# Kernel tuning notes

Hardware: AMD Instinct MI355X
Metric: run time of the kernel (lower is better)

## Reference

```python
import jax, jax.numpy as jnp
import numpy as np

LAYERS = 3  # LightGCN propagation depth per graph


def lgconv(h, edge_index, n_nodes):
    """PyG LGConv: symmetric-normalized aggregation, no self-loops."""
    src, dst = edge_index[0], edge_index[1]
    deg = jax.ops.segment_sum(jnp.ones(dst.shape[0], h.dtype), dst, num_segments=n_nodes)
    dinv = jnp.where(deg > 0, jax.lax.rsqrt(jnp.maximum(deg, 1e-12)), 0.0).astype(h.dtype)
    norm = dinv[src] * dinv[dst]                 # [E]
    msg = h[src] * norm[:, None]                 # [E, D]
    return jax.ops.segment_sum(msg, dst, num_segments=n_nodes)


def setup_inputs() -> dict:
    key = jax.random.key(0)
    ks = jax.random.split(key, 8)
    N, D, E, B, U = 100000, 64, 1200000, 4096, 20000
    return {
        "user": jax.random.randint(ks[0], (B,), 0, U),
        "item": jax.random.randint(ks[1], (B,), 0, N),
        "x": jnp.arange(N),
        "edge_index_0": jax.random.randint(ks[2], (2, E), 0, N),
        "edge_index_1": jax.random.randint(ks[3], (2, E), 0, N),
        "edge_index_2": jax.random.randint(ks[4], (2, E), 0, N),
        "emb_table": jax.random.normal(ks[5], (N, D), jnp.float32),
        "W": jax.random.normal(ks[6], (D, D), jnp.float32),
        "a": jax.random.normal(ks[7], (D, 1), jnp.float32),
    }


def reference(user, item, x, edge_index_0, edge_index_1, edge_index_2, emb_table, W, a):
    n_nodes = emb_table.shape[0]
    ls = []
    for ei in (edge_index_0, edge_index_1, edge_index_2):
        h = emb_table[x]                         # [N, D] embedding lookup
        for _ in range(LAYERS):
            h = lgconv(h, ei, n_nodes)
        ls.append(h)
    emb = jnp.stack(ls, axis=-2)                 # [N, G, D]
    score = (emb @ W) @ a                        # [N, G, 1]
    wgt = jax.nn.softmax(score, axis=-2)         # softmax over channels
    node = jnp.sum(wgt * emb, axis=-2)           # [N, D]
    out = jnp.sum(node[user] * node[item], axis=1)  # [B]
    return out
```

## Files before the change

kernel.cpp:

```cpp
#include <hip/hip_runtime.h>
#include <math.h>

#define PCHUNK 2048
#define CAP 16384

__device__ inline float wave_sum(float v) {
#pragma unroll
    for (int off = 32; off > 0; off >>= 1)
        v += __shfl_xor(v, off, 64);
    return v;
}


__global__ void k_part(const int* __restrict__ e0, const int* __restrict__ e1,
                       const int* __restrict__ e2, int* __restrict__ bcur,
                       int* __restrict__ edata, int E, int NBUC) {
    int g = blockIdx.y;
    const int* ei = (g == 0) ? e0 : (g == 1) ? e1 : e2;
    const int* src = ei;
    const int* dst = ei + E;
    int* bc = bcur + g * 128;
    int* ed = edata + (size_t)g * NBUC * CAP;

    __shared__ int hist[128];
    __shared__ int wcur[128];
    int t = threadIdx.x;
    if (t < 128) hist[t] = 0;
    __syncthreads();

    int ebase = blockIdx.x * PCHUNK;
    int dreg[8];
    bool have[8];
#pragma unroll
    for (int r = 0; r < 8; ++r) {
        int e = ebase + r * 256 + t;
        have[r] = (e < E);
        dreg[r] = have[r] ? dst[e] : 0;
        if (have[r]) atomicAdd(&hist[dreg[r] >> 10], 1);
    }
    __syncthreads();
    if (t < NBUC) {
        int h = hist[t];
        int base = (h > 0) ? atomicAdd(&bc[t], h) : 0;
        wcur[t] = t * CAP + base;
    }
    __syncthreads();
#pragma unroll
    for (int r = 0; r < 8; ++r) {
        if (have[r]) {
            int e = ebase + r * 256 + t;
            int b = dreg[r] >> 10;
            int pos = atomicAdd(&wcur[b], 1);
            if (pos < (b + 1) * CAP)
                ed[pos] = src[e] | ((dreg[r] & 1023) << 20);
        }
    }
}

__global__ void k_bscan(const int* __restrict__ bcur, int* __restrict__ boff,
                        int* __restrict__ offs, int N, int E, int NBUC) {
    int t = threadIdx.x;
    if (t < 3) {
        const int* c = bcur + t * 128;
        int* bo = boff + t * (NBUC + 1);
        int acc = 0;
        for (int b = 0; b < NBUC; ++b) { bo[b] = acc; acc += c[b]; }
        bo[NBUC] = acc;
        offs[(size_t)t * (N + 1) + N] = E;
    }
}

__global__ void k_flag3(const int* __restrict__ user, const int* __restrict__ item,
                        int* __restrict__ flag3, int B) {
    int b = blockIdx.x * blockDim.x + threadIdx.x;
    if (b < B) {
        flag3[user[b]] = 1;
        flag3[item[b]] = 1;
    }
}

__global__ void k_bucket2(const int* __restrict__ edata, const int* __restrict__ bcur,
                          const int* __restrict__ boff, const int* __restrict__ flag3,
                          int* __restrict__ flag2, int* __restrict__ offs,
                          float* __restrict__ dinv, int* __restrict__ perm,
                          int N, int E, int NBUC) {
    int g = blockIdx.y;
    int b = blockIdx.x;
    const int* ed = edata + ((size_t)g * NBUC + b) * CAP;
    int cnt = bcur[g * 128 + b];
    int base = boff[g * (NBUC + 1) + b];
    int* of = offs + (size_t)g * (N + 1);
    float* dv = dinv + (size_t)g * N;
    int* pm = perm + (size_t)g * E;
    int* f2 = flag2 + (size_t)g * N;

    __shared__ int lcnt[1024];
    __shared__ int part[256];
    int t = threadIdx.x;
    int nbase = b << 10;
    for (int i = t; i < 1024; i += 256) lcnt[i] = 0;
    __syncthreads();

    for (int j = t; j < cnt; j += 256)
        atomicAdd(&lcnt[((unsigned)ed[j]) >> 20], 1);
    __syncthreads();

    int i4 = t << 2;
    int c0 = lcnt[i4], c1 = lcnt[i4 + 1], c2 = lcnt[i4 + 2], c3 = lcnt[i4 + 3];
    int tot = c0 + c1 + c2 + c3;
    part[t] = tot;
    __syncthreads();
#pragma unroll
    for (int d = 1; d < 256; d <<= 1) {
        int v = (t >= d) ? part[t - d] : 0;
        __syncthreads();
        part[t] += v;
        __syncthreads();
    }
    int excl = part[t] - tot;
    int cc[4] = {c0, c1, c2, c3};
    int pp[4] = {excl, excl + c0, excl + c0 + c1, excl + c0 + c1 + c2};
#pragma unroll
    for (int k = 0; k < 4; ++k) {
        int n = nbase + i4 + k;
        if (n < N) {
            of[n] = base + pp[k];
            dv[n] = (cc[k] > 0) ? (float)(1.0 / sqrt((double)cc[k])) : 0.0f;
        }
        lcnt[i4 + k] = base + pp[k];
    }
    __syncthreads();
    for (int j = t; j < cnt; j += 256) {
        int v = ed[j];
        int li = ((unsigned)v) >> 20;
        int s = v & 0xFFFFF;
        int pos = atomicAdd(&lcnt[li], 1);
        pm[pos] = s;
        if (flag3[nbase + li]) f2[s] = 1;
    }
}


__global__ void k_gather1(const float* __restrict__ emb, const int* __restrict__ xmap,
                          const int* __restrict__ perm, const int* __restrict__ offs,
                          const float* __restrict__ dinv,
                          float* __restrict__ o0, float* __restrict__ o1,
                          float* __restrict__ o2, int N, int E) {
    int g = blockIdx.y;
    const int* pg = perm + (size_t)g * E;
    const int* og = offs + (size_t)g * (N + 1);
    const float* dg = dinv + (size_t)g * N;
    float* out = (g == 0) ? o0 : (g == 1) ? o1 : o2;

    int n = blockIdx.x * (blockDim.x >> 4) + (threadIdx.x >> 4);
    if (n >= N) return;
    int ql = threadIdx.x & 15;
    int j0 = og[n], j1 = og[n + 1];
    const float4* h4 = (const float4*)emb;
    float ax = 0.f, ay = 0.f, az = 0.f, aw = 0.f;
#pragma unroll 4
    for (int j = j0; j < j1; ++j) {
        int s = pg[j];
        float w = dg[s];
        int row = xmap[s];
        float4 v = h4[(size_t)row * 16 + ql];
        ax += w * v.x; ay += w * v.y; az += w * v.z; aw += w * v.w;
    }
    float wd = dg[n];
    ((float4*)out)[(size_t)n * 16 + ql] = make_float4(ax * wd, ay * wd, az * wd, aw * wd);
}

__global__ void k_gatherP(const float* __restrict__ i0, const float* __restrict__ i1,
                          const float* __restrict__ i2, const int* __restrict__ flagbase,
                          int flagstride, const int* __restrict__ perm,
                          const int* __restrict__ offs, const float* __restrict__ dinv,
                          float* __restrict__ o0, float* __restrict__ o1,
                          float* __restrict__ o2, int N, int E, int gbase) {
    int g = gbase + blockIdx.y;
    const float* hin = (g == 0) ? i0 : (g == 1) ? i1 : i2;
    float* outp = (g == 0) ? o0 : (g == 1) ? o1 : o2;
    const int* flag = flagbase + (size_t)blockIdx.y * flagstride;
    const int* pg = perm + (size_t)g * E;
    const int* og = offs + (size_t)g * (N + 1);
    const float* dg = dinv + (size_t)g * N;

    int n = blockIdx.x * (blockDim.x >> 4) + (threadIdx.x >> 4);
    if (n >= N) return;
    if (!flag[n]) return;
    int ql = threadIdx.x & 15;
    int j0 = og[n], j1 = og[n + 1];
    const float4* h4 = (const float4*)hin;
    float ax = 0.f, ay = 0.f, az = 0.f, aw = 0.f;
#pragma unroll 4
    for (int j = j0; j < j1; ++j) {
        int s = pg[j];
        float w = dg[s];
        float4 v = h4[(size_t)s * 16 + ql];
        ax += w * v.x; ay += w * v.y; az += w * v.z; aw += w * v.w;
    }
    float wd = dg[n];
    ((float4*)outp)[(size_t)n * 16 + ql] = make_float4(ax * wd, ay * wd, az * wd, aw * wd);
}


__device__ inline float node_val(const float* __restrict__ l0, const float* __restrict__ l1,
                                 const float* __restrict__ l2, size_t base, float w) {
    float e0 = l0[base], e1 = l1[base], e2 = l2[base];
    float s0 = wave_sum(e0 * w);
    float s1 = wave_sum(e1 * w);
    float s2 = wave_sum(e2 * w);
    float m = fmaxf(fmaxf(s0, s1), s2);
    float x0 = expf(s0 - m), x1 = expf(s1 - m), x2 = expf(s2 - m);
    return (x0 * e0 + x1 * e1 + x2 * e2) / (x0 + x1 + x2);
}

__global__ void k_score(const int* __restrict__ user, const int* __restrict__ item,
                        const float* __restrict__ l0, const float* __restrict__ l1,
                        const float* __restrict__ l2, const float* __restrict__ W,
                        const float* __restrict__ a, float* __restrict__ out, int B) {
    int lane = threadIdx.x & 63;
    float w = 0.0f;
#pragma unroll
    for (int j = 0; j < 64; ++j) w += W[lane * 64 + j] * a[j];
    int b = blockIdx.x * (blockDim.x >> 6) + (threadIdx.x >> 6);
    if (b >= B) return;
    float nu = node_val(l0, l1, l2, (size_t)user[b] * 64 + lane, w);
    float ni = node_val(l0, l1, l2, (size_t)item[b] * 64 + lane, w);
    float p = wave_sum(nu * ni);
    if (lane == 0) out[b] = p;
}

extern "C" void kernel_launch(void* const* d_in, const int* in_sizes, int n_in,
                              void* d_out, int out_size, void* d_ws, size_t ws_size,
                              hipStream_t stream) {
    const int* user = (const int*)d_in[0];
    const int* item = (const int*)d_in[1];
    const int* x    = (const int*)d_in[2];
    const int* ei[3] = {(const int*)d_in[3], (const int*)d_in[4], (const int*)d_in[5]};
    const float* emb = (const float*)d_in[6];
    const float* W   = (const float*)d_in[7];
    const float* a   = (const float*)d_in[8];
    float* out = (float*)d_out;

    const int B = in_sizes[0];
    const int N = in_sizes[2];
    const int E = in_sizes[3] / 2;
    const int NBUC = (N + 1023) >> 10;

    size_t ND = (size_t)N * 64;
    size_t nint = 384 + (size_t)4 * N + 3 * (size_t)(N + 1) + 3 * (NBUC + 1) + 3 * (size_t)E;
    size_t needBig = (6 * ND + 3 * (size_t)N + nint) * 4 + 1024;
    bool big = (ws_size >= needBig);

    float* fws = (float*)d_ws;
    float* l0   = fws;
    float* l1   = l0 + ND;
    float* l2   = l1 + ND;
    float* t0   = l2 + ND;
    float* t1   = big ? t0 + ND : t0;
    float* t2   = big ? t1 + ND : t0;
    float* dinv = (big ? t2 : t0) + ND;
    int* bcur  = (int*)(dinv + (size_t)3 * N);
    int* flag3 = bcur + 3 * 128;
    int* flag2 = flag3 + N;
    int* offs  = flag2 + (size_t)3 * N;
    int* boff  = offs + (size_t)3 * (N + 1);
    int* perm  = boff + 3 * (NBUC + 1);
    int* edata = (int*)l1;
    float* lbuf[3] = {l0, l1, l2};

    const int pblk = (E + PCHUNK - 1) / PCHUNK;
    const int ngrid = (N + 15) / 16;

    hipMemsetAsync(bcur, 0, ((size_t)384 + (size_t)4 * N) * sizeof(int), stream);

    k_flag3<<<(B + 255) / 256, 256, 0, stream>>>(user, item, flag3, B);
    k_part<<<dim3(pblk, 3), 256, 0, stream>>>(ei[0], ei[1], ei[2], bcur, edata, E, NBUC);
    k_bscan<<<1, 64, 0, stream>>>(bcur, boff, offs, N, E, NBUC);
    k_bucket2<<<dim3(NBUC, 3), 256, 0, stream>>>(edata, bcur, boff, flag3, flag2,
                                                 offs, dinv, perm, N, E, NBUC);

    k_gather1<<<dim3(ngrid, 3), 256, 0, stream>>>(emb, x, perm, offs, dinv,
                                                  l0, l1, l2, N, E);

    if (big) {
        k_gatherP<<<dim3(ngrid, 3), 256, 0, stream>>>(l0, l1, l2, flag2, N,
                                                      perm, offs, dinv,
                                                      t0, t1, t2, N, E, 0);
        k_gatherP<<<dim3(ngrid, 3), 256, 0, stream>>>(t0, t1, t2, flag3, 0,
                                                      perm, offs, dinv,
                                                      l0, l1, l2, N, E, 0);
    } else {
        for (int g = 0; g < 3; ++g) {
            k_gatherP<<<dim3(ngrid, 1), 256, 0, stream>>>(lbuf[g], lbuf[g], lbuf[g],
                                                          flag2 + (size_t)g * N, 0,
                                                          perm, offs, dinv,
                                                          t0, t0, t0, N, E, g);
            k_gatherP<<<dim3(ngrid, 1), 256, 0, stream>>>(t0, t0, t0, flag3, 0,
                                                          perm, offs, dinv,
                                                          lbuf[g], lbuf[g], lbuf[g],
                                                          N, E, g);
        }
    }

    k_score<<<(B + 3) / 4, 256, 0, stream>>>(user, item, l0, l1, l2, W, a, out, B);
}
```

Baseline: 449.9 us.

## Compact flagged nodes into lists and gather only over active nodes

```diff
diff --git a/kernel.cpp b/kernel.cpp
--- a/kernel.cpp
+++ b/kernel.cpp
@@ -70,12 +70,20 @@
     }
 }
 
-__global__ void k_flag3(const int* __restrict__ user, const int* __restrict__ item,
-                        int* __restrict__ flag3, int B) {
+__global__ void k_flag3w(const int* __restrict__ user, const int* __restrict__ item,
+                         int* __restrict__ flag3, const float* __restrict__ W,
+                         const float* __restrict__ a, float* __restrict__ wa, int B) {
     int b = blockIdx.x * blockDim.x + threadIdx.x;
     if (b < B) {
         flag3[user[b]] = 1;
         flag3[item[b]] = 1;
+    }
+    if (blockIdx.x == 0 && threadIdx.x < 64) {
+        int i = threadIdx.x;
+        float acc = 0.0f;
+#pragma unroll
+        for (int j = 0; j < 64; ++j) acc += W[i * 64 + j] * a[j];
+        wa[i] = acc;
     }
 }
 
@@ -140,6 +148,22 @@
     }
 }
 
+__global__ void k_lists(const int* __restrict__ flag2, const int* __restrict__ flag3,
+                        int* __restrict__ list2, int* __restrict__ list3,
+                        int* __restrict__ cnts, int N) {
+    int g = blockIdx.y;
+    int n = blockIdx.x * blockDim.x + threadIdx.x;
+    if (n >= N) return;
+    if (flag2[(size_t)g * N + n]) {
+        int p = atomicAdd(&cnts[g], 1);
+        list2[(size_t)g * N + p] = n;
+    }
+    if (g == 0 && flag3[n]) {
+        int p = atomicAdd(&cnts[3], 1);
+        list3[p] = n;
+    }
+}
+
 
 __global__ void k_gather1(const float* __restrict__ emb, const int* __restrict__ xmap,
                           const int* __restrict__ perm, const int* __restrict__ offs,
@@ -170,36 +194,29 @@
     ((float4*)out)[(size_t)n * 16 + ql] = make_float4(ax * wd, ay * wd, az * wd, aw * wd);
 }
 
-__global__ void k_gatherP(const float* __restrict__ i0, const float* __restrict__ i1,
-                          const float* __restrict__ i2, const int* __restrict__ flagbase,
-                          int flagstride, const int* __restrict__ perm,
-                          const int* __restrict__ offs, const float* __restrict__ dinv,
-                          float* __restrict__ o0, float* __restrict__ o1,
-                          float* __restrict__ o2, int N, int E, int gbase) {
-    int g = gbase + blockIdx.y;
-    const float* hin = (g == 0) ? i0 : (g == 1) ? i1 : i2;
-    float* outp = (g == 0) ? o0 : (g == 1) ? o1 : o2;
-    const int* flag = flagbase + (size_t)blockIdx.y * flagstride;
-    const int* pg = perm + (size_t)g * E;
-    const int* og = offs + (size_t)g * (N + 1);
-    const float* dg = dinv + (size_t)g * N;
-
-    int n = blockIdx.x * (blockDim.x >> 4) + (threadIdx.x >> 4);
-    if (n >= N) return;
-    if (!flag[n]) return;
+__global__ void k_gatherL(const float* __restrict__ hin, const int* __restrict__ list,
+                          const int* __restrict__ cntp, const int* __restrict__ pg,
+                          const int* __restrict__ og, const float* __restrict__ dg,
+                          float* __restrict__ out, int N) {
+    int cnt = *cntp;
+    int groups = (gridDim.x * blockDim.x) >> 4;
+    int gidx = (blockIdx.x * blockDim.x + threadIdx.x) >> 4;
     int ql = threadIdx.x & 15;
-    int j0 = og[n], j1 = og[n + 1];
     const float4* h4 = (const float4*)hin;
-    float ax = 0.f, ay = 0.f, az = 0.f, aw = 0.f;
+    for (int i = gidx; i < cnt; i += groups) {
+        int n = list[i];
+        int j0 = og[n], j1 = og[n + 1];
+        float ax = 0.f, ay = 0.f, az = 0.f, aw = 0.f;
 #pragma unroll 4
-    for (int j = j0; j < j1; ++j) {
-        int s = pg[j];
-        float w = dg[s];
-        float4 v = h4[(size_t)s * 16 + ql];
-        ax += w * v.x; ay += w * v.y; az += w * v.z; aw += w * v.w;
-    }
-    float wd = dg[n];
-    ((float4*)outp)[(size_t)n * 16 + ql] = make_float4(ax * wd, ay * wd, az * wd, aw * wd);
+        for (int j = j0; j < j1; ++j) {
+            int s = pg[j];
+            float w = dg[s];
+            float4 v = h4[(size_t)s * 16 + ql];
+            ax += w * v.x; ay += w * v.y; az += w * v.z; aw += w * v.w;
+        }
+        float wd = dg[n];
+        ((float4*)out)[(size_t)n * 16 + ql] = make_float4(ax * wd, ay * wd, az * wd, aw * wd);
+    }
 }
 
 
@@ -216,12 +233,10 @@
 
 __global__ void k_score(const int* __restrict__ user, const int* __restrict__ item,
                         const float* __restrict__ l0, const float* __restrict__ l1,
-                        const float* __restrict__ l2, const float* __restrict__ W,
-                        const float* __restrict__ a, float* __restrict__ out, int B) {
+                        const float* __restrict__ l2, const float* __restrict__ wa,
+                        float* __restrict__ out, int B) {
     int lane = threadIdx.x & 63;
-    float w = 0.0f;
-#pragma unroll
-    for (int j = 0; j < 64; ++j) w += W[lane * 64 + j] * a[j];
+    float w = wa[lane];
     int b = blockIdx.x * (blockDim.x >> 6) + (threadIdx.x >> 6);
     if (b >= B) return;
     float nu = node_val(l0, l1, l2, (size_t)user[b] * 64 + lane, w);
@@ -248,60 +263,50 @@
     const int NBUC = (N + 1023) >> 10;
 
     size_t ND = (size_t)N * 64;
-    size_t nint = 384 + (size_t)4 * N + 3 * (size_t)(N + 1) + 3 * (NBUC + 1) + 3 * (size_t)E;
-    size_t needBig = (6 * ND + 3 * (size_t)N + nint) * 4 + 1024;
-    bool big = (ws_size >= needBig);
-
     float* fws = (float*)d_ws;
     float* l0   = fws;
     float* l1   = l0 + ND;
     float* l2   = l1 + ND;
     float* t0   = l2 + ND;
-    float* t1   = big ? t0 + ND : t0;
-    float* t2   = big ? t1 + ND : t0;
-    float* dinv = (big ? t2 : t0) + ND;
-    int* bcur  = (int*)(dinv + (size_t)3 * N);
-    int* flag3 = bcur + 3 * 128;
+    float* dinv = t0 + ND;
+    float* wa   = dinv + (size_t)3 * N;
+    int* bcur  = (int*)(wa + 64);
+    int* cnts  = bcur + 3 * 128;
+    int* flag3 = cnts + 128;
     int* flag2 = flag3 + N;
-    int* offs  = flag2 + (size_t)3 * N;
+    int* list3 = flag2 + (size_t)3 * N;
+    int* list2 = list3 + N;
+    int* offs  = list2 + (size_t)3 * N;
     int* boff  = offs + (size_t)3 * (N + 1);
     int* perm  = boff + 3 * (NBUC + 1);
     int* edata = (int*)l1;
     float* lbuf[3] = {l0, l1, l2};
 
     const int pblk = (E + PCHUNK - 1) / PCHUNK;
+    const int nblk = (N + 255) / 256;
     const int ngrid = (N + 15) / 16;
 
-    hipMemsetAsync(bcur, 0, ((size_t)384 + (size_t)4 * N) * sizeof(int), stream);
-
-    k_flag3<<<(B + 255) / 256, 256, 0, stream>>>(user, item, flag3, B);
+    hipMemsetAsync(bcur, 0, ((size_t)512 + (size_t)4 * N) * sizeof(int), stream);
+
+    k_flag3w<<<(B + 255) / 256, 256, 0, stream>>>(user, item, flag3, W, a, wa, B);
     k_part<<<dim3(pblk, 3), 256, 0, stream>>>(ei[0], ei[1], ei[2], bcur, edata, E, NBUC);
     k_bscan<<<1, 64, 0, stream>>>(bcur, boff, offs, N, E, NBUC);
     k_bucket2<<<dim3(NBUC, 3), 256, 0, stream>>>(edata, bcur, boff, flag3, flag2,
                                                  offs, dinv, perm, N, E, NBUC);
+    k_lists<<<dim3(nblk, 3), 256, 0, stream>>>(flag2, flag3, list2, list3, cnts, N);
 
     k_gather1<<<dim3(ngrid, 3), 256, 0, stream>>>(emb, x, perm, offs, dinv,
                                                   l0, l1, l2, N, E);
 
-    if (big) {
-        k_gatherP<<<dim3(ngrid, 3), 256, 0, stream>>>(l0, l1, l2, flag2, N,
-                                                      perm, offs, dinv,
-                                                      t0, t1, t2, N, E, 0);
-        k_gatherP<<<dim3(ngrid, 3), 256, 0, stream>>>(t0, t1, t2, flag3, 0,
-                                                      perm, offs, dinv,
-                                                      l0, l1, l2, N, E, 0);
-    } else {
-        for (int g = 0; g < 3; ++g) {
-            k_gatherP<<<dim3(ngrid, 1), 256, 0, stream>>>(lbuf[g], lbuf[g], lbuf[g],
-                                                          flag2 + (size_t)g * N, 0,
-                                                          perm, offs, dinv,
-                                                          t0, t0, t0, N, E, g);
-            k_gatherP<<<dim3(ngrid, 1), 256, 0, stream>>>(t0, t0, t0, flag3, 0,
-                                                          perm, offs, dinv,
-                                                          lbuf[g], lbuf[g], lbuf[g],
-                                                          N, E, g);
-        }
-    }
-
-    k_score<<<(B + 3) / 4, 256, 0, stream>>>(user, item, l0, l1, l2, W, a, out, B);
-}
+    for (int g = 0; g < 3; ++g) {
+        const int* pg = perm + (size_t)g * E;
+        const int* og = offs + (size_t)g * (N + 1);
+        const float* dg = dinv + (size_t)g * N;
+        k_gatherL<<<1024, 256, 0, stream>>>(lbuf[g], list2 + (size_t)g * N, cnts + g,
+                                            pg, og, dg, t0, N);
+        k_gatherL<<<1024, 256, 0, stream>>>(t0, list3, cnts + 3,
+                                            pg, og, dg, lbuf[g], N);
+    }
+
+    k_score<<<(B + 3) / 4, 256, 0, stream>>>(user, item, l0, l1, l2, wa, out, B);
+}
```

Measured after the change: 534.2 us. 18.7% more time.
